# Optimization experiments

Measured on AMD Instinct MI355X. Metric: run time of the kernel, lower is better.

## Reference

```python
import jax, jax.numpy as jnp
import numpy as np

TOP_K = 5
EPS = 1e-12  # F.normalize eps

def _l2_normalize(v):
    n = jnp.linalg.norm(v, axis=-1, keepdims=True)
    return v / jnp.maximum(n, EPS)

def setup_inputs() -> dict:
    key = jax.random.key(0)
    k1, k2 = jax.random.split(key)
    B, S, C, M = 4, 2048, 512, 32768
    x = jax.random.normal(k1, (B, S, C), dtype=jnp.float32)
    # xavier_uniform-ish init for the memory table
    bound = np.sqrt(6.0 / (M + C)).astype(np.float32)
    memory_mean = jax.random.uniform(k2, (M, C), dtype=jnp.float32, minval=-bound, maxval=bound)
    return {"x": x, "memory_mean": memory_mean}

def reference(x, memory_mean):
    B, S, C = x.shape
    Mmat = memory_mean  # deterministic=True -> _sample_M returns memory_mean
    q = x.reshape(-1, C)                      # [BS, C]
    qn = _l2_normalize(q)
    mn = _l2_normalize(Mmat)                  # [M, C]
    sim = qn @ mn.T                           # [BS, M] cosine similarity
    scores, idx = jax.lax.top_k(sim, TOP_K)   # [BS, K]
    w = jax.nn.softmax(scores, axis=-1)       # [BS, K]
    gathered = Mmat[idx]                      # [BS, K, C]
    retrieved = jnp.einsum('bk,bkc->bc', w, gathered).reshape(B, S, C)
    out = x + 0.5 * retrieved
    return out
```

## Files before the change

### kernel.cpp

```cpp
#include <hip/hip_runtime.h>
#include <math.h>

using f32x4 = __attribute__((ext_vector_type(4))) float;
typedef __attribute__((ext_vector_type(4))) int i32x4;
typedef __attribute__((ext_vector_type(8))) int i32x8;
typedef unsigned char u8;

#define BS    8192
#define CDIM  512
#define MROWS 32768
#define NC    8
#define CHUNK (MROWS / NC)
#define TN    32
#define TQ    128
#define KTOP  5
#define ITERS (CHUNK / TN)
#define ROWB  512
#define KEY_INIT 0x3FFF8000u
#define SCL   0x7F7F7F7F

__device__ __forceinline__ unsigned enc_key(float s, int n) {
    unsigned u = __float_as_uint(s);
    u ^= (unsigned)((int)u >> 31) | 0x80000000u;
    return (u & 0xFFFF8000u) | (unsigned)n;
}
__device__ __forceinline__ float dec_score(unsigned k) {
    unsigned u = k & 0xFFFF8000u;
    u = (u & 0x80000000u) ? (u ^ 0x80000000u) : ~u;
    return __uint_as_float(u);
}

__device__ __forceinline__ void ins_nb(unsigned (&ks)[KTOP], unsigned k) {
    unsigned t = k;
#pragma unroll
    for (int j = 0; j < KTOP; ++j) {
        unsigned hi = t > ks[j] ? t : ks[j];
        unsigned lo = t > ks[j] ? ks[j] : t;
        ks[j] = hi; t = lo;
    }
}

__device__ __forceinline__ float dpp_fmax16(float x) {
    int t;
    t = __builtin_amdgcn_update_dpp(0, __float_as_int(x), 0xB1, 0xF, 0xF, true);
    x = fmaxf(x, __int_as_float(t));
    t = __builtin_amdgcn_update_dpp(0, __float_as_int(x), 0x4E, 0xF, 0xF, true);
    x = fmaxf(x, __int_as_float(t));
    t = __builtin_amdgcn_update_dpp(0, __float_as_int(x), 0x141, 0xF, 0xF, true);
    x = fmaxf(x, __int_as_float(t));
    t = __builtin_amdgcn_update_dpp(0, __float_as_int(x), 0x140, 0xF, 0xF, true);
    x = fmaxf(x, __int_as_float(t));
    return x;
}

__global__ void nrm_cast2(const float* __restrict__ memM, u8* __restrict__ mn,
                          const float* __restrict__ x, u8* __restrict__ qn) {
    int wave = threadIdx.x >> 6, lane = threadIdx.x & 63;
    int row = blockIdx.x * 4 + wave;
    const float* in;
    u8* out;
    if (row < MROWS) { in = memM + (size_t)row * CDIM; out = mn + (size_t)row * ROWB; }
    else             { int r = row - MROWS; in = x + (size_t)r * CDIM; out = qn + (size_t)r * ROWB; }
    const float* rp = in + lane * 8;
    float4 v0 = *(const float4*)rp;
    float4 v1 = *(const float4*)(rp + 4);
    float ss = v0.x * v0.x + v0.y * v0.y + v0.z * v0.z + v0.w * v0.w
             + v1.x * v1.x + v1.y * v1.y + v1.z * v1.z + v1.w * v1.w;
#pragma unroll
    for (int d = 1; d < 64; d <<= 1) ss += __shfl_xor(ss, d);
    float sc = 1.0f / fmaxf(sqrtf(ss), 1e-12f);
    int lo = __builtin_amdgcn_cvt_pk_fp8_f32(v0.x * sc, v0.y * sc, 0, false);
    lo     = __builtin_amdgcn_cvt_pk_fp8_f32(v0.z * sc, v0.w * sc, lo, true);
    int hi = __builtin_amdgcn_cvt_pk_fp8_f32(v1.x * sc, v1.y * sc, 0, false);
    hi     = __builtin_amdgcn_cvt_pk_fp8_f32(v1.z * sc, v1.w * sc, hi, true);
    uint2 o; o.x = (unsigned)lo; o.y = (unsigned)hi;
    *(uint2*)(out + lane * 8) = o;
}

__device__ __forceinline__ void stage_tile(const u8* __restrict__ mn, int nb,
                                           u8* buf, int wave, int lane) {
    const int r0 = wave * 8;
    const int li = lane & 31, half = lane >> 5;
#pragma unroll
    for (int j = 0; j < 4; ++j) {
        const int row = r0 + 2 * j + half;
        const u8* src = mn + (size_t)(nb + row) * ROWB + ((li ^ (row & 7)) * 16);
        __builtin_amdgcn_global_load_lds(
            (const __attribute__((address_space(1))) void*)src,
            (__attribute__((address_space(3))) void*)(buf + (r0 + 2 * j) * ROWB),
            16, 0, 0);
    }
}

__global__ __launch_bounds__(256, 2) void simtopk(
        const u8* __restrict__ qn, const u8* __restrict__ mn,
        unsigned* __restrict__ cand) {
    __shared__ __align__(16) u8 Bt[2][TN * ROWB];

    const int tid  = threadIdx.x;
    const int wave = tid >> 6, lane = tid & 63;
    const int quad = lane >> 4, c16 = lane & 15;
    const int nc = blockIdx.x;
    const int qt = blockIdx.y;
    const int qw = qt * TQ + wave * 32;
    const int nb0 = nc * CHUNK;

    i32x8 a[2][4];
#pragma unroll
    for (int s = 0; s < 2; ++s) {
        const u8* p = qn + (size_t)(qw + s * 16 + c16) * ROWB + quad * 32;
#pragma unroll
        for (int t = 0; t < 4; ++t) {
            i32x4 lo = *(const i32x4*)(p + t * 128);
            i32x4 hi = *(const i32x4*)(p + t * 128 + 16);
            a[s][t] = __builtin_shufflevector(lo, hi, 0, 1, 2, 3, 4, 5, 6, 7);
        }
    }

    unsigned keys[8][KTOP];
    float thr[8];
#pragma unroll
    for (int l = 0; l < 8; ++l) {
        thr[l] = -2.0f;
#pragma unroll
        for (int j = 0; j < KTOP; ++j) keys[l][j] = KEY_INIT;
    }

    const int sw  = c16 & 7;
    const int pb0 = c16 * ROWB + (((2 * quad) ^ sw) * 16);

    stage_tile(mn, nb0, &Bt[0][0], wave, lane);

    for (int it = 0; it < ITERS; ++it) {
        __syncthreads();
        if (it + 1 < ITERS)
            stage_tile(mn, nb0 + (it + 1) * TN, &Bt[(it + 1) & 1][0], wave, lane);

        const u8* bb = &Bt[it & 1][0];
        f32x4 acc00 = {0.f, 0.f, 0.f, 0.f}, acc01 = {0.f, 0.f, 0.f, 0.f};
        f32x4 acc10 = {0.f, 0.f, 0.f, 0.f}, acc11 = {0.f, 0.f, 0.f, 0.f};
#pragma unroll
        for (int t = 0; t < 4; ++t) {
            i32x4 l0 = *(const i32x4*)(bb + pb0 + t * 128);
            i32x4 h0 = *(const i32x4*)(bb + (pb0 ^ 16) + t * 128);
            i32x8 b0 = __builtin_shufflevector(l0, h0, 0, 1, 2, 3, 4, 5, 6, 7);
            acc00 = __builtin_amdgcn_mfma_scale_f32_16x16x128_f8f6f4(
                        a[0][t], b0, acc00, 0, 0, 0, SCL, 0, SCL);
            acc10 = __builtin_amdgcn_mfma_scale_f32_16x16x128_f8f6f4(
                        a[1][t], b0, acc10, 0, 0, 0, SCL, 0, SCL);
            i32x4 l1 = *(const i32x4*)(bb + pb0 + 16 * ROWB + t * 128);
            i32x4 h1 = *(const i32x4*)(bb + (pb0 ^ 16) + 16 * ROWB + t * 128);
            i32x8 b1 = __builtin_shufflevector(l1, h1, 0, 1, 2, 3, 4, 5, 6, 7);
            acc01 = __builtin_amdgcn_mfma_scale_f32_16x16x128_f8f6f4(
                        a[0][t], b1, acc01, 0, 0, 0, SCL, 0, SCL);
            acc11 = __builtin_amdgcn_mfma_scale_f32_16x16x128_f8f6f4(
                        a[1][t], b1, acc11, 0, 0, 0, SCL, 0, SCL);
        }

        const int nb = nb0 + it * TN;
        const int n0 = nb + c16, n1 = nb + 16 + c16;
#pragma unroll
        for (int j = 0; j < 4; ++j) {
            if (acc00[j] > thr[j])     ins_nb(keys[j],     enc_key(acc00[j], n0));
            if (acc01[j] > thr[j])     ins_nb(keys[j],     enc_key(acc01[j], n1));
            if (acc10[j] > thr[4 + j]) ins_nb(keys[4 + j], enc_key(acc10[j], n0));
            if (acc11[j] > thr[4 + j]) ins_nb(keys[4 + j], enc_key(acc11[j], n1));
        }
        if ((it & 3) == 3) {
#pragma unroll
            for (int l = 0; l < 8; ++l)
                thr[l] = dpp_fmax16(fmaxf(thr[l], dec_score(keys[l][KTOP - 1])));
        }
    }

#pragma unroll
    for (int d = 1; d <= 8; d <<= 1) {
#pragma unroll
        for (int l = 0; l < 8; ++l) {
            unsigned rk[KTOP];
#pragma unroll
            for (int j = 0; j < KTOP; ++j) rk[j] = (unsigned)__shfl_xor((int)keys[l][j], d);
#pragma unroll
            for (int j = 0; j < KTOP; ++j) ins_nb(keys[l], rk[j]);
        }
    }

#pragma unroll
    for (int l = 0; l < 8; ++l) {
        if (c16 == l) {
            const int q = qw + (l >> 2) * 16 + quad * 4 + (l & 3);
            unsigned* cp = cand + ((size_t)q * NC + nc) * KTOP;
#pragma unroll
            for (int j = 0; j < KTOP; ++j) cp[j] = keys[l][j];
        }
    }
}

__global__ void epilogue(const float* __restrict__ x, const float* __restrict__ mem,
                         const unsigned* __restrict__ cand, float* __restrict__ out) {
    int wave = threadIdx.x >> 6, lane = threadIdx.x & 63;
    int q = blockIdx.x * 4 + wave;

    unsigned key = (lane < NC * KTOP) ? cand[(size_t)q * (NC * KTOP) + lane] : 0u;
    float s[KTOP]; int id[KTOP];
#pragma unroll
    for (int k = 0; k < KTOP; ++k) {
        unsigned m = key;
#pragma unroll
        for (int d = 32; d; d >>= 1) {
            unsigned o = (unsigned)__shfl_xor((int)m, d);
            m = o > m ? o : m;
        }
        s[k] = dec_score(m);
        id[k] = (int)(m & 0x7FFFu);
        unsigned long long b = __ballot(key == m);
        int first = __ffsll((long long)b) - 1;
        if (lane == first) key = 0u;
    }
    float w[KTOP], sum = 0.f;
#pragma unroll
    for (int k = 0; k < KTOP; ++k) { w[k] = expf(s[k] - s[0]); sum += w[k]; }
    float inv = 0.5f / sum;

    int c = lane * 8;
    const float4* xp = (const float4*)(x + (size_t)q * CDIM + c);
    float4 o0 = xp[0], o1 = xp[1];
#pragma unroll
    for (int k = 0; k < KTOP; ++k) {
        float wk = w[k] * inv;
        const float4* mp = (const float4*)(mem + (size_t)id[k] * CDIM + c);
        float4 g0 = mp[0], g1 = mp[1];
        o0.x += wk * g0.x; o0.y += wk * g0.y; o0.z += wk * g0.z; o0.w += wk * g0.w;
        o1.x += wk * g1.x; o1.y += wk * g1.y; o1.z += wk * g1.z; o1.w += wk * g1.w;
    }
    float* op = out + (size_t)q * CDIM + c;
    *(float4*)op = o0;
    *(float4*)(op + 4) = o1;
}

extern "C" void kernel_launch(void* const* d_in, const int* in_sizes, int n_in,
                              void* d_out, int out_size, void* d_ws, size_t ws_size,
                              hipStream_t stream) {
    const float* x    = (const float*)d_in[0];
    const float* memM = (const float*)d_in[1];
    float* out = (float*)d_out;

    u8* mn = (u8*)d_ws;
    u8* qn = mn + (size_t)MROWS * ROWB;
    unsigned* cand = (unsigned*)(qn + (size_t)BS * ROWB);

    nrm_cast2<<<(MROWS + BS) / 4, 256, 0, stream>>>(memM, mn, x, qn);
    simtopk<<<dim3(NC, BS / TQ), 256, 0, stream>>>(qn, mn, cand);
    epilogue<<<BS / 4, 256, 0, stream>>>(x, memM, cand, out);
}
```

Measured before the change: 343.8 us.

## Drop LDS staging; load memory tiles directly into registers with software-pipelined top-k

Removes the shared-memory double buffer and the per-iteration block barrier. Each wave now loads its 16-row memory tile straight from global into registers. The tile width drops from 32 to 16 rows, and the top-k insertion for the previous tile's scores is deferred by one step so it overlaps the current tile's MFMAs. The threshold refresh interval doubles in steps so it stays the same in rows. The cost is that the four waves of a block no longer share loads, so global and L2 traffic for the memory table rises and each load goes through the cache without swizzled LDS reuse.

```diff
diff --git a/kernel.cpp b/kernel.cpp
--- a/kernel.cpp
+++ b/kernel.cpp
@@ -11,10 +11,10 @@
 #define MROWS 32768
 #define NC    8
 #define CHUNK (MROWS / NC)
-#define TN    32
+#define TN    16
 #define TQ    128
 #define KTOP  5
-#define ITERS (CHUNK / TN)
+#define STEPS (CHUNK / TN)
 #define ROWB  512
 #define KEY_INIT 0x3FFF8000u
 #define SCL   0x7F7F7F7F
@@ -77,26 +77,9 @@
     *(uint2*)(out + lane * 8) = o;
 }
 
-__device__ __forceinline__ void stage_tile(const u8* __restrict__ mn, int nb,
-                                           u8* buf, int wave, int lane) {
-    const int r0 = wave * 8;
-    const int li = lane & 31, half = lane >> 5;
-#pragma unroll
-    for (int j = 0; j < 4; ++j) {
-        const int row = r0 + 2 * j + half;
-        const u8* src = mn + (size_t)(nb + row) * ROWB + ((li ^ (row & 7)) * 16);
-        __builtin_amdgcn_global_load_lds(
-            (const __attribute__((address_space(1))) void*)src,
-            (__attribute__((address_space(3))) void*)(buf + (r0 + 2 * j) * ROWB),
-            16, 0, 0);
-    }
-}
-
 __global__ __launch_bounds__(256, 2) void simtopk(
         const u8* __restrict__ qn, const u8* __restrict__ mn,
         unsigned* __restrict__ cand) {
-    __shared__ __align__(16) u8 Bt[2][TN * ROWB];
-
     const int tid  = threadIdx.x;
     const int wave = tid >> 6, lane = tid & 63;
     const int quad = lane >> 4, c16 = lane & 15;
@@ -126,51 +109,48 @@
         for (int j = 0; j < KTOP; ++j) keys[l][j] = KEY_INIT;
     }
 
-    const int sw  = c16 & 7;
-    const int pb0 = c16 * ROWB + (((2 * quad) ^ sw) * 16);
-
-    stage_tile(mn, nb0, &Bt[0][0], wave, lane);
-
-    for (int it = 0; it < ITERS; ++it) {
-        __syncthreads();
-        if (it + 1 < ITERS)
-            stage_tile(mn, nb0 + (it + 1) * TN, &Bt[(it + 1) & 1][0], wave, lane);
-
-        const u8* bb = &Bt[it & 1][0];
-        f32x4 acc00 = {0.f, 0.f, 0.f, 0.f}, acc01 = {0.f, 0.f, 0.f, 0.f};
-        f32x4 acc10 = {0.f, 0.f, 0.f, 0.f}, acc11 = {0.f, 0.f, 0.f, 0.f};
+    const u8* pB = mn + (size_t)(nb0 + c16) * ROWB + quad * 32;
+
+    f32x4 p0 = {-2.f, -2.f, -2.f, -2.f}, p1 = p0;
+    int np = nb0;
+
+    for (int it = 0; it < STEPS; ++it) {
+        f32x4 acc0 = {0.f, 0.f, 0.f, 0.f}, acc1 = {0.f, 0.f, 0.f, 0.f};
+        i32x8 b[4];
 #pragma unroll
         for (int t = 0; t < 4; ++t) {
-            i32x4 l0 = *(const i32x4*)(bb + pb0 + t * 128);
-            i32x4 h0 = *(const i32x4*)(bb + (pb0 ^ 16) + t * 128);
-            i32x8 b0 = __builtin_shufflevector(l0, h0, 0, 1, 2, 3, 4, 5, 6, 7);
-            acc00 = __builtin_amdgcn_mfma_scale_f32_16x16x128_f8f6f4(
-                        a[0][t], b0, acc00, 0, 0, 0, SCL, 0, SCL);
-            acc10 = __builtin_amdgcn_mfma_scale_f32_16x16x128_f8f6f4(
-                        a[1][t], b0, acc10, 0, 0, 0, SCL, 0, SCL);
-            i32x4 l1 = *(const i32x4*)(bb + pb0 + 16 * ROWB + t * 128);
-            i32x4 h1 = *(const i32x4*)(bb + (pb0 ^ 16) + 16 * ROWB + t * 128);
-            i32x8 b1 = __builtin_shufflevector(l1, h1, 0, 1, 2, 3, 4, 5, 6, 7);
-            acc01 = __builtin_amdgcn_mfma_scale_f32_16x16x128_f8f6f4(
-                        a[0][t], b1, acc01, 0, 0, 0, SCL, 0, SCL);
-            acc11 = __builtin_amdgcn_mfma_scale_f32_16x16x128_f8f6f4(
-                        a[1][t], b1, acc11, 0, 0, 0, SCL, 0, SCL);
-        }
-
-        const int nb = nb0 + it * TN;
-        const int n0 = nb + c16, n1 = nb + 16 + c16;
+            i32x4 lo = *(const i32x4*)(pB + t * 128);
+            i32x4 hi = *(const i32x4*)(pB + t * 128 + 16);
+            b[t] = __builtin_shufflevector(lo, hi, 0, 1, 2, 3, 4, 5, 6, 7);
+        }
+#pragma unroll
+        for (int t = 0; t < 4; ++t) {
+            acc0 = __builtin_amdgcn_mfma_scale_f32_16x16x128_f8f6f4(
+                       a[0][t], b[t], acc0, 0, 0, 0, SCL, 0, SCL);
+            acc1 = __builtin_amdgcn_mfma_scale_f32_16x16x128_f8f6f4(
+                       a[1][t], b[t], acc1, 0, 0, 0, SCL, 0, SCL);
+        }
+
 #pragma unroll
         for (int j = 0; j < 4; ++j) {
-            if (acc00[j] > thr[j])     ins_nb(keys[j],     enc_key(acc00[j], n0));
-            if (acc01[j] > thr[j])     ins_nb(keys[j],     enc_key(acc01[j], n1));
-            if (acc10[j] > thr[4 + j]) ins_nb(keys[4 + j], enc_key(acc10[j], n0));
-            if (acc11[j] > thr[4 + j]) ins_nb(keys[4 + j], enc_key(acc11[j], n1));
-        }
-        if ((it & 3) == 3) {
+            if (p0[j] > thr[j])     ins_nb(keys[j],     enc_key(p0[j], np));
+            if (p1[j] > thr[4 + j]) ins_nb(keys[4 + j], enc_key(p1[j], np));
+        }
+        if ((it & 7) == 7) {
 #pragma unroll
             for (int l = 0; l < 8; ++l)
                 thr[l] = dpp_fmax16(fmaxf(thr[l], dec_score(keys[l][KTOP - 1])));
         }
+
+        p0 = acc0; p1 = acc1;
+        np = nb0 + it * TN + c16;
+        pB += TN * ROWB;
+    }
+
+#pragma unroll
+    for (int j = 0; j < 4; ++j) {
+        if (p0[j] > thr[j])     ins_nb(keys[j],     enc_key(p0[j], np));
+        if (p1[j] > thr[4 + j]) ins_nb(keys[4 + j], enc_key(p1[j], np));
     }
 
 #pragma unroll
```

Result: slower. 580.6 us (+68.9%).
